# Performance work log

Hardware: AMD Instinct MI355X
Metric: run time of the kernel (lower is better)

The kernel has to match this reference:

```python
import jax, jax.numpy as jnp
import numpy as np

N_NODES = 100000
N_EDGES = 1600000
LEAKY_SLOPE = 0.01


def _degrees(src, dst, n):
    ones = jnp.ones(src.shape[0], dtype=jnp.float32)
    out_deg = jax.ops.segment_sum(ones, src, num_segments=n)
    in_deg = jax.ops.segment_sum(ones, dst, num_segments=n)
    # DGL clamps degree to min 1 to avoid inf norms
    return jnp.maximum(out_deg, 1.0), jnp.maximum(in_deg, 1.0)


def graph_conv(x, W, b, src, dst, out_deg, in_deg):
    # DGL GraphConv, norm='both': h = D_in^{-1/2} A^T (D_out^{-1/2} x W) + b
    h = x * jax.lax.rsqrt(out_deg)[:, None]          # [N, Fin]
    h = h @ W                                        # [N, Fout] (linear first; math-equivalent)
    agg = jax.ops.segment_sum(h[src], dst, num_segments=x.shape[0])  # sparse neighbor sum
    return agg * jax.lax.rsqrt(in_deg)[:, None] + b


def setup_inputs() -> dict:
    key = jax.random.key(0)
    ks = jax.random.split(key, 9)
    d_in, h0, h1, d_out = 128, 128, 64, 64
    return {
        "n_feat": jax.random.normal(ks[0], (N_NODES, d_in), dtype=jnp.float32),
        "src": jax.random.randint(ks[1], (N_EDGES,), 0, N_NODES),
        "dst": jax.random.randint(ks[2], (N_EDGES,), 0, N_NODES),
        "W0": jax.random.normal(ks[3], (d_in, h0), dtype=jnp.float32) / np.sqrt(d_in),
        "b0": jnp.zeros((h0,), dtype=jnp.float32),
        "W1": jax.random.normal(ks[4], (h0, h1), dtype=jnp.float32) / np.sqrt(h0),
        "b1": jnp.zeros((h1,), dtype=jnp.float32),
        "W2": jax.random.normal(ks[5], (h1, d_out), dtype=jnp.float32) / np.sqrt(h1),
        "b2": jnp.zeros((d_out,), dtype=jnp.float32),
    }


def reference(n_feat, src, dst, W0, b0, W1, b1, W2, b2):
    out_deg, in_deg = _degrees(src, dst, n_feat.shape[0])
    lrelu = lambda h: jnp.where(h >= 0, h, LEAKY_SLOPE * h)
    h = n_feat.reshape(n_feat.shape[0], -1)  # Flatten
    h = lrelu(graph_conv(h, W0, b0, src, dst, out_deg, in_deg))
    h = lrelu(graph_conv(h, W1, b1, src, dst, out_deg, in_deg))
    h = lrelu(graph_conv(h, W2, b2, src, dst, out_deg, in_deg))
    return h
```

## Files before the change

kernel.cpp:

```cpp
#include <hip/hip_runtime.h>
#include <hip/hip_fp16.h>

#define NN 100000
#define NE 1600000

#define HG 128
#define HSLICE (NE / HG)
#define PB (NN / 4)

typedef _Float16 half8 __attribute__((ext_vector_type(8)));
typedef float floatx4 __attribute__((ext_vector_type(4)));
typedef unsigned int uint4n __attribute__((ext_vector_type(4)));
typedef float float4n __attribute__((ext_vector_type(4)));
typedef unsigned char u8;

__device__ __forceinline__ float lrelu(float x) { return x >= 0.f ? x : 0.01f * x; }


__global__ __launch_bounds__(1024) void k_hist(const int* __restrict__ src, const int* __restrict__ dst,
                                               u8* __restrict__ occ, u8* __restrict__ icc,
                                               u8* __restrict__ rk) {
    __shared__ int lh[PB];
    int tid = threadIdx.x;
    int b = blockIdx.x;
    bool isDst = b < HG;
    int c = isDst ? b : b - HG;
    const int* __restrict__ key = isDst ? dst : src;
    u8* __restrict__ outArr = isDst ? icc : occ;
    for (int j = tid; j < PB; j += 1024) lh[j] = 0;
    __syncthreads();
    int e0 = c * HSLICE;
    for (int e = e0 + tid; e < e0 + HSLICE; e += 1024) {
        int k = key[e];
        int sh = (k & 3) * 8;
        int old = atomicAdd(&lh[k >> 2], 1 << sh);
        if (isDst) rk[e] = (u8)((old >> sh) & 255);
    }
    __syncthreads();
    int* dst4 = (int*)&outArr[(size_t)c * NN];
    for (int j = tid; j < PB; j += 1024) dst4[j] = lh[j];
}

__global__ __launch_bounds__(256) void k_reduce(const u8* __restrict__ occ, u8* __restrict__ icc,
                                                int* __restrict__ ic, float* __restrict__ ro,
                                                float* __restrict__ ri, int* __restrict__ bsums) {
    int i = blockIdx.x * 256 + threadIdx.x;
    int run = 0;
    if (i < NN) {
        int so = 0;
#pragma unroll 8
        for (int c = 0; c < HG; c++) so += occ[(size_t)c * NN + i];
#pragma unroll 8
        for (int c = 0; c < HG; c++) {
            int v = icc[(size_t)c * NN + i];
            icc[(size_t)c * NN + i] = (u8)run;
            run += v;
        }
        ic[i] = run;
        ro[i] = rsqrtf((float)(so > 1 ? so : 1));
        ri[i] = rsqrtf((float)(run > 1 ? run : 1));
    }
    int v = run;
#pragma unroll
    for (int s = 32; s > 0; s >>= 1) v += __shfl_down(v, s, 64);
    __shared__ int ws[4];
    int lane = threadIdx.x & 63, wid = threadIdx.x >> 6;
    if (lane == 0) ws[wid] = v;
    __syncthreads();
    if (threadIdx.x == 0) bsums[blockIdx.x] = ws[0] + ws[1] + ws[2] + ws[3];
}

__global__ __launch_bounds__(256) void k_scan_f(const int* __restrict__ cnt, const int* __restrict__ bsums,
                                                int* __restrict__ off) {
    int tid = threadIdx.x;
    int idx = blockIdx.x * 256 + tid;
    int lane = tid & 63, wid = tid >> 6;
    __shared__ int ws[4];
    __shared__ int wbase[4];
    __shared__ int base_s;
    int pb = 0;
    for (int j = tid; j < blockIdx.x; j += 256) pb += bsums[j];
#pragma unroll
    for (int s = 32; s > 0; s >>= 1) pb += __shfl_down(pb, s, 64);
    if (lane == 0) ws[wid] = pb;
    __syncthreads();
    if (tid == 0) base_s = ws[0] + ws[1] + ws[2] + ws[3];
    __syncthreads();
    int v = (idx < NN) ? cnt[idx] : 0;
    int x = v;
#pragma unroll
    for (int s = 1; s < 64; s <<= 1) { int t = __shfl_up(x, s, 64); if (lane >= s) x += t; }
    if (lane == 63) ws[wid] = x;
    __syncthreads();
    if (tid == 0) {
        wbase[0] = 0;
        wbase[1] = ws[0];
        wbase[2] = ws[0] + ws[1];
        wbase[3] = ws[0] + ws[1] + ws[2];
    }
    __syncthreads();
    if (idx <= NN) off[idx] = base_s + wbase[wid] + x - v;
}

__global__ __launch_bounds__(256) void k_fill(const int* __restrict__ src, const int* __restrict__ dst,
                                              const int* __restrict__ off, const u8* __restrict__ icc,
                                              const u8* __restrict__ rk, int* __restrict__ col) {
    int i = blockIdx.x * 256 + threadIdx.x;
    if (i >= NE) return;
    int d = __builtin_nontemporal_load(&dst[i]);
    int c = i / HSLICE;
    int pos = off[d] + (int)icc[(size_t)c * NN + d] + (int)__builtin_nontemporal_load(&rk[i]);
    col[pos] = __builtin_nontemporal_load(&src[i]);
}


template <int K, int N, typename AT>
__global__ __launch_bounds__(256) void k_gemm(const AT* __restrict__ A, const float* __restrict__ W,
                                              const float* __restrict__ rsq, __half* __restrict__ C, int M) {
    constexpr int KP = K + 8;
    constexpr int NT = N / 16;
    constexpr int KT = K / 32;
    __shared__ _Float16 Wh[N * KP];
    __shared__ _Float16 Wl[N * KP];
    int tid = threadIdx.x;
    for (int idx = tid; idx < K * N; idx += 256) {
        int k = idx / N, n = idx - k * N;
        float w = W[idx];
        _Float16 wh = (_Float16)w;
        _Float16 wl = (_Float16)((w - (float)wh) * 1024.0f);
        Wh[n * KP + k] = wh;
        Wl[n * KP + k] = wl;
    }
    __syncthreads();

    int wv = tid >> 6, l = tid & 63;
    int m = l & 15, quad = l >> 4;
    int row = blockIdx.x * 64 + wv * 16 + m;
    float r = (row < M) ? rsq[row] : 0.f;

    half8 ah[KT], al[KT];
#pragma unroll
    for (int c = 0; c < KT; c++) {
        int k0 = c * 32 + quad * 8;
        float av[8];
        if (row < M) {
            if constexpr (sizeof(AT) == 2) {
                union { uint4n u; half8 h; } raw;
                raw.u = *(const uint4n*)&A[(size_t)row * K + k0];
#pragma unroll
                for (int j = 0; j < 8; j++) av[j] = (float)raw.h[j] * r;
            } else {
                float4n f0 = *(const float4n*)&A[(size_t)row * K + k0];
                float4n f1 = *(const float4n*)&A[(size_t)row * K + k0 + 4];
                av[0] = f0.x * r; av[1] = f0.y * r; av[2] = f0.z * r; av[3] = f0.w * r;
                av[4] = f1.x * r; av[5] = f1.y * r; av[6] = f1.z * r; av[7] = f1.w * r;
            }
        } else {
#pragma unroll
            for (int j = 0; j < 8; j++) av[j] = 0.f;
        }
#pragma unroll
        for (int j = 0; j < 8; j++) {
            _Float16 h = (_Float16)av[j];
            ah[c][j] = h;
            al[c][j] = (_Float16)(av[j] - (float)h);
        }
    }

    int crow0 = blockIdx.x * 64 + wv * 16 + quad * 4;
#pragma unroll
    for (int nn = 0; nn < NT; nn++) {
        floatx4 accA = {0.f, 0.f, 0.f, 0.f};
        floatx4 accB = {0.f, 0.f, 0.f, 0.f};
#pragma unroll
        for (int c = 0; c < KT; c++) {
            int boff = (nn * 16 + m) * KP + c * 32 + quad * 8;
            half8 bh = *(const half8*)&Wh[boff];
            half8 bl = *(const half8*)&Wl[boff];
            accA = __builtin_amdgcn_mfma_f32_16x16x32_f16(ah[c], bh, accA, 0, 0, 0);
            accA = __builtin_amdgcn_mfma_f32_16x16x32_f16(al[c], bh, accA, 0, 0, 0);
            accB = __builtin_amdgcn_mfma_f32_16x16x32_f16(ah[c], bl, accB, 0, 0, 0);
        }
#pragma unroll
        for (int i = 0; i < 4; i++) {
            int rr = crow0 + i;
            if (rr < M) C[(size_t)rr * N + nn * 16 + m] =
                __float2half_rn(accA[i] + accB[i] * (1.f / 1024.f));
        }
    }
}


__device__ __forceinline__ void acc8(float* a, uint4n u) {
    union { uint4n u; __half2 h2[4]; } v;
    v.u = u;
#pragma unroll
    for (int j = 0; j < 4; j++) {
        float2 f = __half22float2(v.h2[j]);
        a[2 * j] += f.x;
        a[2 * j + 1] += f.y;
    }
}

template <int F, typename OutT>
__global__ __launch_bounds__(256) void k_agg(const __half* __restrict__ h, const int* __restrict__ col,
                                             const int* __restrict__ off, const float* __restrict__ rsqi,
                                             const float* __restrict__ bias, OutT* __restrict__ out) {
    constexpr int TPN = F / 8;
    constexpr int ES = 2;
    constexpr int TG = TPN * ES;
    int t = blockIdx.x * 256 + threadIdx.x;
    int node = t / TG;
    int sub = t % TG;
    int g = sub / TPN;
    int lane = sub % TPN;
    int e0 = off[node], e1 = off[node + 1];
    float acc[8] = {};
    const __half* hp = h + 8 * lane;
    int e = e0 + g;
    for (; e + 7 * ES < e1; e += 8 * ES) {
        int s[8];
#pragma unroll
        for (int j = 0; j < 8; j++) s[j] = __builtin_nontemporal_load(&col[e + j * ES]);
        uint4n v[8];
#pragma unroll
        for (int j = 0; j < 8; j++) v[j] = *(const uint4n*)(hp + (size_t)s[j] * F);
#pragma unroll
        for (int j = 0; j < 8; j++) acc8(acc, v[j]);
    }
    for (; e + 3 * ES < e1; e += 4 * ES) {
        int s0 = __builtin_nontemporal_load(&col[e]);
        int s1 = __builtin_nontemporal_load(&col[e + ES]);
        int s2 = __builtin_nontemporal_load(&col[e + 2 * ES]);
        int s3 = __builtin_nontemporal_load(&col[e + 3 * ES]);
        uint4n v0 = *(const uint4n*)(hp + (size_t)s0 * F);
        uint4n v1 = *(const uint4n*)(hp + (size_t)s1 * F);
        uint4n v2 = *(const uint4n*)(hp + (size_t)s2 * F);
        uint4n v3 = *(const uint4n*)(hp + (size_t)s3 * F);
        acc8(acc, v0); acc8(acc, v1); acc8(acc, v2); acc8(acc, v3);
    }
    for (; e < e1; e += ES) {
        int s = __builtin_nontemporal_load(&col[e]);
        acc8(acc, *(const uint4n*)(hp + (size_t)s * F));
    }
#pragma unroll
    for (int j = 0; j < 8; j++) acc[j] += __shfl_xor(acc[j], TPN, 64);
    if (g != 0) return;
    float r = rsqi[node];
    float o[8];
#pragma unroll
    for (int j = 0; j < 8; j++) o[j] = lrelu(acc[j] * r + bias[8 * lane + j]);
    if constexpr (sizeof(OutT) == 4) {
        float4n o0 = {o[0], o[1], o[2], o[3]};
        float4n o1 = {o[4], o[5], o[6], o[7]};
        __builtin_nontemporal_store(o0, (float4n*)&out[(size_t)node * F + 8 * lane]);
        __builtin_nontemporal_store(o1, (float4n*)&out[(size_t)node * F + 8 * lane + 4]);
    } else {
        union { uint4n u; __half2 h2[4]; } pk;
#pragma unroll
        for (int j = 0; j < 4; j++) {
            pk.h2[j].x = __float2half_rn(o[2 * j]);
            pk.h2[j].y = __float2half_rn(o[2 * j + 1]);
        }
        __builtin_nontemporal_store(pk.u, (uint4n*)&out[(size_t)node * F + 8 * lane]);
    }
}


extern "C" void kernel_launch(void* const* d_in, const int* in_sizes, int n_in,
                              void* d_out, int out_size, void* d_ws, size_t ws_size,
                              hipStream_t stream) {
    const float* x   = (const float*)d_in[0];
    const int*   src = (const int*)d_in[1];
    const int*   dst = (const int*)d_in[2];
    const float* W0  = (const float*)d_in[3];
    const float* b0  = (const float*)d_in[4];
    const float* W1  = (const float*)d_in[5];
    const float* b1  = (const float*)d_in[6];
    const float* W2  = (const float*)d_in[7];
    const float* b2  = (const float*)d_in[8];

    char* w = (char*)d_ws;
    int*    col = (int*)(w);
    int*    off = (int*)(w + 6400000);
    int*    ic  = (int*)(w + 6800128);
    int*    bs  = (int*)(w + 7200128);
    float*  ro  = (float*)(w + 7202176);
    float*  ri  = (float*)(w + 7602176);

    u8* occ = (u8*)(w + 8002176);
    u8* icc = (u8*)(w + 20802176);
    u8* rk  = (u8*)(w + 33602176);

    __half* bufA = (__half*)(w + 8002176);
    __half* bufB = (__half*)(w + 33602176);

    if (ws_size < (size_t)59202176) return;

    k_hist<<<2 * HG, 1024, 0, stream>>>(src, dst, occ, icc, rk);
    int nb = (NN + 255) / 256;
    k_reduce<<<nb, 256, 0, stream>>>(occ, icc, ic, ro, ri, bs);
    k_scan_f<<<nb, 256, 0, stream>>>(ic, bs, off);
    k_fill<<<(NE + 255) / 256, 256, 0, stream>>>(src, dst, off, icc, rk, col);

    int gb = (NN + 63) / 64;
    k_gemm<128, 128, float><<<gb, 256, 0, stream>>>(x, W0, ro, bufA, NN);
    k_agg<128, __half><<<12500, 256, 0, stream>>>(bufA, col, off, ri, b0, bufB);
    k_gemm<128, 64, __half><<<gb, 256, 0, stream>>>(bufB, W1, ro, bufA, NN);
    k_agg<64, __half><<<6250, 256, 0, stream>>>(bufA, col, off, ri, b1, bufB);
    k_gemm<64, 64, __half><<<gb, 256, 0, stream>>>(bufB, W2, ro, bufA, NN);
    k_agg<64, float><<<6250, 256, 0, stream>>>(bufA, col, off, ri, b2, (float*)d_out);
}
```

Before: 392.4 us.

## Fuse CSR-build kernels into one persistent kernel with grid barriers

```diff
diff --git a/kernel.cpp b/kernel.cpp
--- a/kernel.cpp
+++ b/kernel.cpp
@@ -7,6 +7,8 @@
 #define HG 128
 #define HSLICE (NE / HG)
 #define PB (NN / 4)
+#define NPB 391
+#define MAGIC 0x5F3C0001
 
 typedef _Float16 half8 __attribute__((ext_vector_type(8)));
 typedef float floatx4 __attribute__((ext_vector_type(4)));
@@ -17,100 +19,131 @@
 __device__ __forceinline__ float lrelu(float x) { return x >= 0.f ? x : 0.01f * x; }
 
 
-__global__ __launch_bounds__(1024) void k_hist(const int* __restrict__ src, const int* __restrict__ dst,
+__device__ __forceinline__ void gbar(int* bar, int r, bool waitInit) {
+    __syncthreads();
+    if (threadIdx.x == 0) {
+        if (waitInit)
+            while (__hip_atomic_load(&bar[32], __ATOMIC_ACQUIRE, __HIP_MEMORY_SCOPE_AGENT) != MAGIC) {}
+        __threadfence();
+        int t = __hip_atomic_fetch_add(&bar[r * 4], 1, __ATOMIC_ACQ_REL, __HIP_MEMORY_SCOPE_AGENT);
+        if (t == 255)
+            __hip_atomic_store(&bar[16 + r * 4], 1, __ATOMIC_RELEASE, __HIP_MEMORY_SCOPE_AGENT);
+        else
+            while (__hip_atomic_load(&bar[16 + r * 4], __ATOMIC_ACQUIRE, __HIP_MEMORY_SCOPE_AGENT) == 0) {}
+        __threadfence();
+    }
+    __syncthreads();
+}
+
+__global__ __launch_bounds__(1024) void k_prep(const int* __restrict__ src, const int* __restrict__ dst,
                                                u8* __restrict__ occ, u8* __restrict__ icc,
-                                               u8* __restrict__ rk) {
+                                               u8* __restrict__ rk, int* __restrict__ ic,
+                                               float* __restrict__ ro, float* __restrict__ ri,
+                                               int* __restrict__ bsums, int* __restrict__ off,
+                                               int* __restrict__ bar, int* __restrict__ col) {
     __shared__ int lh[PB];
-    int tid = threadIdx.x;
-    int b = blockIdx.x;
-    bool isDst = b < HG;
-    int c = isDst ? b : b - HG;
-    const int* __restrict__ key = isDst ? dst : src;
-    u8* __restrict__ outArr = isDst ? icc : occ;
-    for (int j = tid; j < PB; j += 1024) lh[j] = 0;
-    __syncthreads();
-    int e0 = c * HSLICE;
-    for (int e = e0 + tid; e < e0 + HSLICE; e += 1024) {
-        int k = key[e];
-        int sh = (k & 3) * 8;
-        int old = atomicAdd(&lh[k >> 2], 1 << sh);
-        if (isDst) rk[e] = (u8)((old >> sh) & 255);
-    }
-    __syncthreads();
-    int* dst4 = (int*)&outArr[(size_t)c * NN];
-    for (int j = tid; j < PB; j += 1024) dst4[j] = lh[j];
-}
-
-__global__ __launch_bounds__(256) void k_reduce(const u8* __restrict__ occ, u8* __restrict__ icc,
-                                                int* __restrict__ ic, float* __restrict__ ro,
-                                                float* __restrict__ ri, int* __restrict__ bsums) {
-    int i = blockIdx.x * 256 + threadIdx.x;
+    const int tid = threadIdx.x;
+    const int b = blockIdx.x;
+    const int lane = tid & 63, wid = tid >> 6;
+
+    if (b == 0 && tid == 0) {
+        for (int r = 0; r < 3; r++) { bar[r * 4] = 0; bar[16 + r * 4] = 0; }
+        __hip_atomic_store(&bar[32], MAGIC, __ATOMIC_RELEASE, __HIP_MEMORY_SCOPE_AGENT);
+    }
+
+    {
+        bool isDst = b < HG;
+        int c = isDst ? b : b - HG;
+        const int* __restrict__ key = isDst ? dst : src;
+        u8* __restrict__ outArr = isDst ? icc : occ;
+        for (int j = tid; j < PB; j += 1024) lh[j] = 0;
+        __syncthreads();
+        int e0 = c * HSLICE;
+        for (int e = e0 + tid; e < e0 + HSLICE; e += 1024) {
+            int k = key[e];
+            int sh = (k & 3) * 8;
+            int old = atomicAdd(&lh[k >> 2], 1 << sh);
+            if (isDst) rk[e] = (u8)((old >> sh) & 255);
+        }
+        __syncthreads();
+        int* dst4 = (int*)&outArr[(size_t)c * NN];
+        for (int j = tid; j < PB; j += 1024) dst4[j] = lh[j];
+    }
+    gbar(bar, 0, true);
+
+    const int n0 = b * NPB;
+    const int n1 = (n0 + NPB < NN) ? n0 + NPB : NN;
     int run = 0;
-    if (i < NN) {
-        int so = 0;
+    {
+        int n = n0 + tid;
+        if (tid < NPB && n < NN) {
+            int so = 0;
 #pragma unroll 8
-        for (int c = 0; c < HG; c++) so += occ[(size_t)c * NN + i];
+            for (int c = 0; c < HG; c++) so += occ[(size_t)c * NN + n];
 #pragma unroll 8
-        for (int c = 0; c < HG; c++) {
-            int v = icc[(size_t)c * NN + i];
-            icc[(size_t)c * NN + i] = (u8)run;
-            run += v;
-        }
-        ic[i] = run;
-        ro[i] = rsqrtf((float)(so > 1 ? so : 1));
-        ri[i] = rsqrtf((float)(run > 1 ? run : 1));
-    }
-    int v = run;
-#pragma unroll
-    for (int s = 32; s > 0; s >>= 1) v += __shfl_down(v, s, 64);
-    __shared__ int ws[4];
-    int lane = threadIdx.x & 63, wid = threadIdx.x >> 6;
-    if (lane == 0) ws[wid] = v;
-    __syncthreads();
-    if (threadIdx.x == 0) bsums[blockIdx.x] = ws[0] + ws[1] + ws[2] + ws[3];
-}
-
-__global__ __launch_bounds__(256) void k_scan_f(const int* __restrict__ cnt, const int* __restrict__ bsums,
-                                                int* __restrict__ off) {
-    int tid = threadIdx.x;
-    int idx = blockIdx.x * 256 + tid;
-    int lane = tid & 63, wid = tid >> 6;
-    __shared__ int ws[4];
-    __shared__ int wbase[4];
-    __shared__ int base_s;
-    int pb = 0;
-    for (int j = tid; j < blockIdx.x; j += 256) pb += bsums[j];
-#pragma unroll
-    for (int s = 32; s > 0; s >>= 1) pb += __shfl_down(pb, s, 64);
-    if (lane == 0) ws[wid] = pb;
-    __syncthreads();
-    if (tid == 0) base_s = ws[0] + ws[1] + ws[2] + ws[3];
-    __syncthreads();
-    int v = (idx < NN) ? cnt[idx] : 0;
-    int x = v;
-#pragma unroll
-    for (int s = 1; s < 64; s <<= 1) { int t = __shfl_up(x, s, 64); if (lane >= s) x += t; }
-    if (lane == 63) ws[wid] = x;
-    __syncthreads();
-    if (tid == 0) {
-        wbase[0] = 0;
-        wbase[1] = ws[0];
-        wbase[2] = ws[0] + ws[1];
-        wbase[3] = ws[0] + ws[1] + ws[2];
-    }
-    __syncthreads();
-    if (idx <= NN) off[idx] = base_s + wbase[wid] + x - v;
-}
-
-__global__ __launch_bounds__(256) void k_fill(const int* __restrict__ src, const int* __restrict__ dst,
-                                              const int* __restrict__ off, const u8* __restrict__ icc,
-                                              const u8* __restrict__ rk, int* __restrict__ col) {
-    int i = blockIdx.x * 256 + threadIdx.x;
-    if (i >= NE) return;
-    int d = __builtin_nontemporal_load(&dst[i]);
-    int c = i / HSLICE;
-    int pos = off[d] + (int)icc[(size_t)c * NN + d] + (int)__builtin_nontemporal_load(&rk[i]);
-    col[pos] = __builtin_nontemporal_load(&src[i]);
+            for (int c = 0; c < HG; c++) {
+                int v = icc[(size_t)c * NN + n];
+                icc[(size_t)c * NN + n] = (u8)run;
+                run += v;
+            }
+            ic[n] = run;
+            ro[n] = rsqrtf((float)(so > 1 ? so : 1));
+            ri[n] = rsqrtf((float)(run > 1 ? run : 1));
+        }
+        int v = run;
+#pragma unroll
+        for (int s = 32; s > 0; s >>= 1) v += __shfl_down(v, s, 64);
+        if (lane == 0) lh[wid] = v;
+        __syncthreads();
+        if (tid == 0) {
+            int t = 0;
+#pragma unroll
+            for (int j = 0; j < 16; j++) t += lh[j];
+            bsums[b] = t;
+        }
+    }
+    gbar(bar, 1, false);
+
+    {
+        int pb = (tid < b) ? bsums[tid] : 0;
+#pragma unroll
+        for (int s = 32; s > 0; s >>= 1) pb += __shfl_down(pb, s, 64);
+        if (lane == 0) lh[64 + wid] = pb;
+        __syncthreads();
+        if (tid == 0) {
+            int t = 0;
+#pragma unroll
+            for (int j = 0; j < 16; j++) t += lh[64 + j];
+            lh[100] = t;
+        }
+        __syncthreads();
+        int base_s = lh[100];
+        int cntn = n1 - n0;
+        int v = (tid < cntn) ? ic[n0 + tid] : 0;
+        int x = v;
+#pragma unroll
+        for (int s = 1; s < 64; s <<= 1) { int t = __shfl_up(x, s, 64); if (lane >= s) x += t; }
+        __syncthreads();
+        if (lane == 63) lh[wid] = x;
+        __syncthreads();
+        if (tid == 0) {
+            int racc = 0;
+#pragma unroll
+            for (int j = 0; j < 16; j++) { int t = lh[j]; lh[16 + j] = racc; racc += t; }
+            lh[101] = racc;
+        }
+        __syncthreads();
+        if (tid < cntn) off[n0 + tid] = base_s + lh[16 + wid] + x - v;
+        if (b == 255 && tid == 0) off[NN] = base_s + lh[101];
+    }
+    gbar(bar, 2, false);
+
+    for (int e = b * 1024 + tid; e < NE; e += 256 * 1024) {
+        int d = __builtin_nontemporal_load(&dst[e]);
+        int c = e / HSLICE;
+        int pos = off[d] + (int)icc[(size_t)c * NN + d] + (int)__builtin_nontemporal_load(&rk[e]);
+        col[pos] = __builtin_nontemporal_load(&src[e]);
+    }
 }
 
 
@@ -202,12 +235,11 @@
     }
 }
 
-template <int F, typename OutT>
+template <int F, int ES, typename OutT>
 __global__ __launch_bounds__(256) void k_agg(const __half* __restrict__ h, const int* __restrict__ col,
                                              const int* __restrict__ off, const float* __restrict__ rsqi,
                                              const float* __restrict__ bias, OutT* __restrict__ out) {
     constexpr int TPN = F / 8;
-    constexpr int ES = 2;
     constexpr int TG = TPN * ES;
     int t = blockIdx.x * 256 + threadIdx.x;
     int node = t / TG;
@@ -218,16 +250,6 @@
     float acc[8] = {};
     const __half* hp = h + 8 * lane;
     int e = e0 + g;
-    for (; e + 7 * ES < e1; e += 8 * ES) {
-        int s[8];
-#pragma unroll
-        for (int j = 0; j < 8; j++) s[j] = __builtin_nontemporal_load(&col[e + j * ES]);
-        uint4n v[8];
-#pragma unroll
-        for (int j = 0; j < 8; j++) v[j] = *(const uint4n*)(hp + (size_t)s[j] * F);
-#pragma unroll
-        for (int j = 0; j < 8; j++) acc8(acc, v[j]);
-    }
     for (; e + 3 * ES < e1; e += 4 * ES) {
         int s0 = __builtin_nontemporal_load(&col[e]);
         int s1 = __builtin_nontemporal_load(&col[e + ES]);
@@ -287,27 +309,24 @@
     int*    bs  = (int*)(w + 7200128);
     float*  ro  = (float*)(w + 7202176);
     float*  ri  = (float*)(w + 7602176);
-
-    u8* occ = (u8*)(w + 8002176);
-    u8* icc = (u8*)(w + 20802176);
-    u8* rk  = (u8*)(w + 33602176);
-
-    __half* bufA = (__half*)(w + 8002176);
-    __half* bufB = (__half*)(w + 33602176);
-
-    if (ws_size < (size_t)59202176) return;
-
-    k_hist<<<2 * HG, 1024, 0, stream>>>(src, dst, occ, icc, rk);
-    int nb = (NN + 255) / 256;
-    k_reduce<<<nb, 256, 0, stream>>>(occ, icc, ic, ro, ri, bs);
-    k_scan_f<<<nb, 256, 0, stream>>>(ic, bs, off);
-    k_fill<<<(NE + 255) / 256, 256, 0, stream>>>(src, dst, off, icc, rk, col);
+    int*    bar = (int*)(w + 8002176);
+
+    u8* occ = (u8*)(w + 8002432);
+    u8* icc = (u8*)(w + 20802432);
+    u8* rk  = (u8*)(w + 33602432);
+
+    __half* bufA = (__half*)(w + 8002432);
+    __half* bufB = (__half*)(w + 33602432);
+
+    if (ws_size < (size_t)59202432) return;
+
+    k_prep<<<256, 1024, 0, stream>>>(src, dst, occ, icc, rk, ic, ro, ri, bs, off, bar, col);
 
     int gb = (NN + 63) / 64;
     k_gemm<128, 128, float><<<gb, 256, 0, stream>>>(x, W0, ro, bufA, NN);
-    k_agg<128, __half><<<12500, 256, 0, stream>>>(bufA, col, off, ri, b0, bufB);
+    k_agg<128, 2, __half><<<12500, 256, 0, stream>>>(bufA, col, off, ri, b0, bufB);
     k_gemm<128, 64, __half><<<gb, 256, 0, stream>>>(bufB, W1, ro, bufA, NN);
-    k_agg<64, __half><<<6250, 256, 0, stream>>>(bufA, col, off, ri, b1, bufB);
+    k_agg<64, 2, __half><<<6250, 256, 0, stream>>>(bufA, col, off, ri, b1, bufB);
     k_gemm<64, 64, __half><<<gb, 256, 0, stream>>>(bufB, W2, ro, bufA, NN);
-    k_agg<64, float><<<6250, 256, 0, stream>>>(bufA, col, off, ri, b2, (float*)d_out);
-}
+    k_agg<64, 2, float><<<6250, 256, 0, stream>>>(bufA, col, off, ri, b2, (float*)d_out);
+}
```

Measured after the change: 483.6 us. 1.23x slower.

## Vectorize degree reduce over packed byte counters and drop 8-wide agg unroll

Applied to the files above, without the earlier changes.

```diff
diff --git a/kernel.cpp b/kernel.cpp
--- a/kernel.cpp
+++ b/kernel.cpp
@@ -7,11 +7,13 @@
 #define HG 128
 #define HSLICE (NE / HG)
 #define PB (NN / 4)
+#define QN (NN / 4)
 
 typedef _Float16 half8 __attribute__((ext_vector_type(8)));
 typedef float floatx4 __attribute__((ext_vector_type(4)));
 typedef unsigned int uint4n __attribute__((ext_vector_type(4)));
 typedef float float4n __attribute__((ext_vector_type(4)));
+typedef int i32x4 __attribute__((ext_vector_type(4)));
 typedef unsigned char u8;
 
 __device__ __forceinline__ float lrelu(float x) { return x >= 0.f ? x : 0.01f * x; }
@@ -44,30 +46,64 @@
 __global__ __launch_bounds__(256) void k_reduce(const u8* __restrict__ occ, u8* __restrict__ icc,
                                                 int* __restrict__ ic, float* __restrict__ ro,
                                                 float* __restrict__ ri, int* __restrict__ bsums) {
-    int i = blockIdx.x * 256 + threadIdx.x;
-    int run = 0;
-    if (i < NN) {
-        int so = 0;
-#pragma unroll 8
-        for (int c = 0; c < HG; c++) so += occ[(size_t)c * NN + i];
-#pragma unroll 8
-        for (int c = 0; c < HG; c++) {
-            int v = icc[(size_t)c * NN + i];
-            icc[(size_t)c * NN + i] = (u8)run;
-            run += v;
-        }
-        ic[i] = run;
-        ro[i] = rsqrtf((float)(so > 1 ? so : 1));
-        ri[i] = rsqrtf((float)(run > 1 ? run : 1));
-    }
-    int v = run;
-#pragma unroll
-    for (int s = 32; s > 0; s >>= 1) v += __shfl_down(v, s, 64);
+    const int tid = threadIdx.x;
+    const int iq = tid & 15;
+    const int j  = (tid >> 4) & 3;
+    const int wv = tid >> 6;
+    const int q  = blockIdx.x * 64 + wv * 16 + iq;
+    const bool valid = q < QN;
+    const int c0 = j * 32;
+    const int* occ4 = (const int*)occ;
+    int* icc4 = (int*)icc;
+    unsigned so = 0, ti = 0;
+    unsigned v[32];
+    if (valid) {
+#pragma unroll
+        for (int c = 0; c < 32; c++) so += (unsigned)occ4[(size_t)(c0 + c) * QN + q];
+#pragma unroll
+        for (int c = 0; c < 32; c++) {
+            v[c] = (unsigned)icc4[(size_t)(c0 + c) * QN + q];
+            ti += v[c];
+        }
+    }
+    unsigned tjA = __shfl(ti, iq, 64);
+    unsigned tjB = __shfl(ti, iq + 16, 64);
+    unsigned tjC = __shfl(ti, iq + 32, 64);
+    unsigned base = (j > 0 ? tjA : 0u) + (j > 1 ? tjB : 0u) + (j > 2 ? tjC : 0u);
+    unsigned tot = ti;
+    tot += __shfl_xor(tot, 16, 64);
+    tot += __shfl_xor(tot, 32, 64);
+    unsigned soa = so;
+    soa += __shfl_xor(soa, 16, 64);
+    soa += __shfl_xor(soa, 32, 64);
+    if (valid) {
+        unsigned run = base;
+#pragma unroll
+        for (int c = 0; c < 32; c++) {
+            icc4[(size_t)(c0 + c) * QN + q] = (int)run;
+            run += v[c];
+        }
+    }
+    int s4 = 0;
+    if (valid && j == 0) {
+        int d0 = tot & 255, d1 = (tot >> 8) & 255, d2 = (tot >> 16) & 255, d3 = tot >> 24;
+        int o0 = soa & 255, o1 = (soa >> 8) & 255, o2 = (soa >> 16) & 255, o3 = soa >> 24;
+        i32x4 icv = {d0, d1, d2, d3};
+        *(i32x4*)&ic[4 * q] = icv;
+        float4n rov = {rsqrtf((float)(o0 > 1 ? o0 : 1)), rsqrtf((float)(o1 > 1 ? o1 : 1)),
+                       rsqrtf((float)(o2 > 1 ? o2 : 1)), rsqrtf((float)(o3 > 1 ? o3 : 1))};
+        *(float4n*)&ro[4 * q] = rov;
+        float4n riv = {rsqrtf((float)(d0 > 1 ? d0 : 1)), rsqrtf((float)(d1 > 1 ? d1 : 1)),
+                       rsqrtf((float)(d2 > 1 ? d2 : 1)), rsqrtf((float)(d3 > 1 ? d3 : 1))};
+        *(float4n*)&ri[4 * q] = riv;
+        s4 = d0 + d1 + d2 + d3;
+    }
+#pragma unroll
+    for (int s = 32; s > 0; s >>= 1) s4 += __shfl_down(s4, s, 64);
     __shared__ int ws[4];
-    int lane = threadIdx.x & 63, wid = threadIdx.x >> 6;
-    if (lane == 0) ws[wid] = v;
-    __syncthreads();
-    if (threadIdx.x == 0) bsums[blockIdx.x] = ws[0] + ws[1] + ws[2] + ws[3];
+    if ((tid & 63) == 0) ws[wv] = s4;
+    __syncthreads();
+    if (tid == 0) bsums[blockIdx.x] = ws[0] + ws[1] + ws[2] + ws[3];
 }
 
 __global__ __launch_bounds__(256) void k_scan_f(const int* __restrict__ cnt, const int* __restrict__ bsums,
@@ -202,12 +238,11 @@
     }
 }
 
-template <int F, typename OutT>
+template <int F, int ES, typename OutT>
 __global__ __launch_bounds__(256) void k_agg(const __half* __restrict__ h, const int* __restrict__ col,
                                              const int* __restrict__ off, const float* __restrict__ rsqi,
                                              const float* __restrict__ bias, OutT* __restrict__ out) {
     constexpr int TPN = F / 8;
-    constexpr int ES = 2;
     constexpr int TG = TPN * ES;
     int t = blockIdx.x * 256 + threadIdx.x;
     int node = t / TG;
@@ -218,16 +253,6 @@
     float acc[8] = {};
     const __half* hp = h + 8 * lane;
     int e = e0 + g;
-    for (; e + 7 * ES < e1; e += 8 * ES) {
-        int s[8];
-#pragma unroll
-        for (int j = 0; j < 8; j++) s[j] = __builtin_nontemporal_load(&col[e + j * ES]);
-        uint4n v[8];
-#pragma unroll
-        for (int j = 0; j < 8; j++) v[j] = *(const uint4n*)(hp + (size_t)s[j] * F);
-#pragma unroll
-        for (int j = 0; j < 8; j++) acc8(acc, v[j]);
-    }
     for (; e + 3 * ES < e1; e += 4 * ES) {
         int s0 = __builtin_nontemporal_load(&col[e]);
         int s1 = __builtin_nontemporal_load(&col[e + ES]);
@@ -305,9 +330,9 @@
 
     int gb = (NN + 63) / 64;
     k_gemm<128, 128, float><<<gb, 256, 0, stream>>>(x, W0, ro, bufA, NN);
-    k_agg<128, __half><<<12500, 256, 0, stream>>>(bufA, col, off, ri, b0, bufB);
+    k_agg<128, 2, __half><<<12500, 256, 0, stream>>>(bufA, col, off, ri, b0, bufB);
     k_gemm<128, 64, __half><<<gb, 256, 0, stream>>>(bufB, W1, ro, bufA, NN);
-    k_agg<64, __half><<<6250, 256, 0, stream>>>(bufA, col, off, ri, b1, bufB);
+    k_agg<64, 2, __half><<<6250, 256, 0, stream>>>(bufA, col, off, ri, b1, bufB);
     k_gemm<64, 64, __half><<<gb, 256, 0, stream>>>(bufB, W2, ro, bufA, NN);
-    k_agg<64, float><<<6250, 256, 0, stream>>>(bufA, col, off, ri, b2, (float*)d_out);
-}
+    k_agg<64, 2, float><<<6250, 256, 0, stream>>>(bufA, col, off, ri, b2, (float*)d_out);
+}
```

Result: faster. 369.2 us (-5.9%).
